# Kernel optimization log

Hardware: AMD Instinct MI355X
Metric: run time of the kernel (lower is better)

## Reference

```python
import jax, jax.numpy as jnp
import numpy as np

EMBED_DIM = 1024
NUM_HEADS = 16
HEAD_DIM = EMBED_DIM // NUM_HEADS
BITS = 8


def quantize_bits(x, bits):
    # Faithful min-max fake quantization from the original module.
    qmax = 2 ** bits - 1
    x_min = x.min()
    x_max = x.max()
    scale = (x_max - x_min) / (qmax + 1e-08)
    x_q = jnp.round(jnp.clip((x - x_min) / (scale + 1e-08), 0, qmax))
    return x_q * scale + x_min


def rope_sin_cos(seq_len, dim):
    # inv_freq over half the head dim, matching RotaryEmbedding's freqs table.
    inv_freq = 1.0 / 10000 ** (jnp.arange(0, dim, 2, dtype=jnp.float32) / dim)
    t = jnp.arange(seq_len, dtype=jnp.float32)
    freqs = t[:, None] * inv_freq[None, :]  # (S, D/2)
    return jnp.sin(freqs), jnp.cos(freqs)


def apply_rotary(x, sin, cos):
    # x: (B, H, S, D); sin/cos: (1, 1, S, D/2)
    x1, x2 = jnp.split(x, 2, axis=-1)
    return jnp.concatenate([x1 * cos - x2 * sin, x1 * sin + x2 * cos], axis=-1)


def setup_inputs() -> dict:
    key = jax.random.key(0)
    k1, k2, k3 = jax.random.split(key, 3)
    B, S, E = 2, 2048, EMBED_DIM
    x = jax.random.normal(k1, (B, S, E), dtype=jnp.float32)
    # lecun_normal-style init: std = 1/sqrt(fan_in)
    w_qkv = jax.random.normal(k2, (E, 3 * E), dtype=jnp.float32) / np.sqrt(E)
    w_out = jax.random.normal(k3, (E, E), dtype=jnp.float32) / np.sqrt(E)
    return {"x": x, "w_qkv": w_qkv, "w_out": w_out}


def reference(x, w_qkv, w_out):
    B, S, E = x.shape
    H, D = NUM_HEADS, HEAD_DIM
    # Fake-quantized QKV projection
    qkv = x @ quantize_bits(w_qkv, BITS)                    # (B, S, 3E)
    qkv = qkv.reshape(B, S, 3, H, D)
    q = qkv[:, :, 0].transpose(0, 2, 1, 3)                  # (B, H, S, D)
    k = qkv[:, :, 1].transpose(0, 2, 1, 3)
    v = qkv[:, :, 2].transpose(0, 2, 1, 3)
    sin, cos = rope_sin_cos(S, D)
    sin = sin[None, None]
    cos = cos[None, None]
    q = apply_rotary(q, sin, cos)
    k = apply_rotary(k, sin, cos)
    scores = jnp.einsum('bhqd,bhkd->bhqk', q, k) / jnp.sqrt(jnp.float32(D))
    attn = jax.nn.softmax(scores, axis=-1)                  # (B, H, S, S)
    out = jnp.einsum('bhqk,bhkd->bhqd', attn, v)            # (B, H, S, D)
    out = out.transpose(0, 2, 1, 3).reshape(B, S, E)
    return out @ quantize_bits(w_out, BITS)
```

## Files before the change

### kernel.cpp

```cpp
#include <hip/hip_runtime.h>
#include <hip/hip_bf16.h>

typedef __bf16 bf16;
typedef bf16  bf16x8 __attribute__((ext_vector_type(8)));
typedef bf16  bf16x4 __attribute__((ext_vector_type(4)));
typedef bf16  bf16x2 __attribute__((ext_vector_type(2)));
typedef float f32x4  __attribute__((ext_vector_type(4)));
typedef float f32x16 __attribute__((ext_vector_type(16)));
typedef int   i32x4  __attribute__((ext_vector_type(4)));

#define MFMA16(a,b,c) __builtin_amdgcn_mfma_f32_16x16x32_bf16((a),(b),(c),0,0,0)
#define MFMA32(a,b,c) __builtin_amdgcn_mfma_f32_32x32x16_bf16((a),(b),(c),0,0,0)

#define GLDS16(gp, lp) __builtin_amdgcn_global_load_lds( \
    (const __attribute__((address_space(1))) void*)(void*)(gp), \
    (__attribute__((address_space(3))) void*)(lp), 16, 0, 0)

static __device__ __forceinline__ bf16x8 lds_frag(const char* p){
  i32x4 v = *(const i32x4*)p;
  return __builtin_bit_cast(bf16x8, v);
}
static __device__ __forceinline__ bf16x8 g_frag(const bf16* p){
  i32x4 v = *(const i32x4*)p;
  return __builtin_bit_cast(bf16x8, v);
}
static __device__ __forceinline__ unsigned pk_bf16(float a, float b){
  bf16x2 v = { (bf16)a, (bf16)b };
  return __builtin_bit_cast(unsigned, v);
}
static __device__ __forceinline__ void p32swap(unsigned &a, unsigned &b){
  asm("v_permlane32_swap_b32 %0, %1" : "+v"(a), "+v"(b));
}

__device__ __forceinline__ unsigned fmap(float f){
  unsigned u = __float_as_uint(f);
  return (u & 0x80000000u) ? ~u : (u | 0x80000000u);
}
__device__ __forceinline__ float funmap(unsigned m){
  unsigned u = (m & 0x80000000u) ? (m & 0x7FFFFFFFu) : ~m;
  return __uint_as_float(u);
}

__global__ void init_mm(unsigned* mm){
  if (threadIdx.x == 0){
    mm[0] = 0xFFFFFFFFu; mm[1] = 0u;
    mm[2] = 0xFFFFFFFFu; mm[3] = 0u;
  }
}

__global__ void minmax_k(const float* __restrict__ w, int n, unsigned* __restrict__ mm){
  __shared__ unsigned smn[256], smx[256];
  int tid = threadIdx.x;
  unsigned lmn = 0xFFFFFFFFu, lmx = 0u;
  for (int i = blockIdx.x * blockDim.x + tid; i < n; i += gridDim.x * blockDim.x){
    unsigned u = fmap(w[i]);
    lmn = min(lmn, u); lmx = max(lmx, u);
  }
  smn[tid] = lmn; smx[tid] = lmx;
  __syncthreads();
  for (int s = 128; s > 0; s >>= 1){
    if (tid < s){
      smn[tid] = min(smn[tid], smn[tid + s]);
      smx[tid] = max(smx[tid], smx[tid + s]);
    }
    __syncthreads();
  }
  if (tid == 0){ atomicMin(&mm[0], smn[0]); atomicMax(&mm[1], smx[0]); }
}

__global__ void dq_t(const float* __restrict__ w, bf16* __restrict__ wt,
                     int R, int C, const unsigned* __restrict__ mm){
  __shared__ float t[32][33];
  float xmin = funmap(mm[0]);
  float xmax = funmap(mm[1]);
  float scale = (xmax - xmin) / 255.0f;
  float denom = scale + 1e-8f;
  int ct = blockIdx.x * 32, rt = blockIdx.y * 32;
  int tx = threadIdx.x, ty = threadIdx.y;
#pragma unroll
  for (int p = 0; p < 4; ++p){
    int r = rt + p * 8 + ty;
    float x = w[(size_t)r * C + ct + tx];
    float q = rintf(fminf(fmaxf((x - xmin) / denom, 0.0f), 255.0f));
    t[p * 8 + ty][tx] = q * scale + xmin;
  }
  __syncthreads();
#pragma unroll
  for (int p = 0; p < 4; ++p){
    int c = p * 8 + ty;
    wt[(size_t)(ct + c) * R + rt + tx] = (bf16)t[tx][c];
  }
}

__global__ void cast_x(const float* __restrict__ x, bf16* __restrict__ xb, int n4){
  int i = blockIdx.x * 256 + threadIdx.x;
  if (i < n4){
    f32x4 v = *(const f32x4*)(x + (size_t)i * 4);
    bf16x4 o = { (bf16)v.x, (bf16)v.y, (bf16)v.z, (bf16)v.w };
    *(bf16x4*)(xb + (size_t)i * 4) = o;
  }
}

__global__ void sincos_k(float2* __restrict__ sctab){
  int idx = blockIdx.x * 256 + threadIdx.x;
  int i = idx & 31, s = idx >> 5;
  float invf = powf(10000.0f, -(float)i / 32.0f);
  float fr = (float)s * invf;
  float2 cs; cs.x = cosf(fr); cs.y = sinf(fr);
  sctab[idx] = cs;
}

__global__ void vtrans_b(const bf16* __restrict__ Vraw, bf16* __restrict__ Vt){
  __shared__ float t[64][65];
  int bh = blockIdx.x >> 5;
  int st = (blockIdx.x & 31) * 64;
  int tx = threadIdx.x & 63, ty4 = threadIdx.x >> 6;
#pragma unroll
  for (int p = 0; p < 16; ++p){
    int s = p * 4 + ty4;
    t[s][tx] = (float)Vraw[((size_t)bh * 2048 + st + s) * 64 + tx];
  }
  __syncthreads();
#pragma unroll
  for (int p = 0; p < 16; ++p){
    int d = p * 4 + ty4;
    Vt[((size_t)bh * 64 + d) * 2048 + st + tx] = (bf16)t[tx][d];
  }
}

__global__ __launch_bounds__(256, 2) void gemm_bt(
    const bf16* __restrict__ A, const bf16* __restrict__ Bt,
    float* __restrict__ C, int M, int N, int K)
{
  __shared__ __align__(16) char lds[32768];
  int nbx = N >> 7;
  int bid = blockIdx.x;
  int nwg = gridDim.x;
  if ((nwg & 7) == 0){ int q = nwg >> 3; bid = (bid & 7) * q + (bid >> 3); }
  int row0 = (bid / nbx) << 7;
  int col0 = (bid % nbx) << 7;
  int tid = threadIdx.x, lane = tid & 63, wid = tid >> 6;
  int wr = (wid >> 1) * 64, wc = (wid & 1) * 64;
  int lr = lane & 15, g = lane >> 4;

  int aoff[2][4], boff[2][4];
#pragma unroll
  for (int kk = 0; kk < 2; ++kk){
#pragma unroll
    for (int m = 0; m < 4; ++m){
      int ra = wr + m * 16 + lr;
      aoff[kk][m] = ra * 128 + ((((kk * 4 + g) ^ ((ra >> 1) & 7))) << 4);
      int rb = wc + m * 16 + lr;
      boff[kk][m] = 16384 + rb * 128 + ((((kk * 4 + g) ^ ((rb >> 1) & 7))) << 4);
    }
  }

  const bf16* pA[4]; const bf16* pB[4]; int loff[4];
#pragma unroll
  for (int is = 0; is < 4; ++is){
    int f = is * 4096 + wid * 1024 + lane * 16;
    int r = f >> 7, c = (f >> 4) & 7;
    int cg = c ^ ((r >> 1) & 7);
    pA[is] = A  + (size_t)(row0 + r) * K + cg * 8;
    pB[is] = Bt + (size_t)(col0 + r) * K + cg * 8;
    loff[is] = is * 4096 + wid * 1024;
  }

  f32x4 acc[4][4] = {};
  for (int kt = 0; kt < K; kt += 64){
    __syncthreads();
#pragma unroll
    for (int is = 0; is < 4; ++is){
      GLDS16(pA[is] + kt, lds + loff[is]);
      GLDS16(pB[is] + kt, lds + 16384 + loff[is]);
    }
    __syncthreads();
#pragma unroll
    for (int kk = 0; kk < 2; ++kk){
      bf16x8 af[4], bfb[4];
#pragma unroll
      for (int m = 0; m < 4; ++m) af[m] = lds_frag(lds + aoff[kk][m]);
#pragma unroll
      for (int n = 0; n < 4; ++n) bfb[n] = lds_frag(lds + boff[kk][n]);
#pragma unroll
      for (int m = 0; m < 4; ++m)
#pragma unroll
        for (int n = 0; n < 4; ++n)
          acc[m][n] = MFMA16(af[m], bfb[n], acc[m][n]);
    }
  }

#pragma unroll
  for (int m = 0; m < 4; ++m){
    int row = row0 + wr + m * 16 + g * 4;
#pragma unroll
    for (int n = 0; n < 4; ++n){
      int col = col0 + wc + n * 16 + lr;
      float* cp = C + (size_t)row * N + col;
#pragma unroll
      for (int r = 0; r < 4; ++r)
        cp[(size_t)r * N] = acc[m][n][r];
    }
  }
}

__global__ __launch_bounds__(256, 2) void gemm_qkv(
    const bf16* __restrict__ A, const bf16* __restrict__ Bt,
    const float2* __restrict__ sctab,
    bf16* __restrict__ Qr, bf16* __restrict__ Kr, bf16* __restrict__ Vraw,
    int M, int N, int K)
{
  __shared__ __align__(16) char lds[32768];
  int nbx = N >> 7;
  int bid = blockIdx.x;
  int nwg = gridDim.x;
  if ((nwg & 7) == 0){ int q = nwg >> 3; bid = (bid & 7) * q + (bid >> 3); }
  int row0 = (bid / nbx) << 7;
  int col0 = (bid % nbx) << 7;
  int tid = threadIdx.x, lane = tid & 63, wid = tid >> 6;
  int wr = (wid >> 1) * 64, wc = (wid & 1) * 64;
  int lr = lane & 15, g = lane >> 4;

  int aoff[2][4], boff[2][4];
#pragma unroll
  for (int kk = 0; kk < 2; ++kk){
#pragma unroll
    for (int m = 0; m < 4; ++m){
      int ra = wr + m * 16 + lr;
      aoff[kk][m] = ra * 128 + ((((kk * 4 + g) ^ ((ra >> 1) & 7))) << 4);
      int rb = wc + m * 16 + lr;
      boff[kk][m] = 16384 + rb * 128 + ((((kk * 4 + g) ^ ((rb >> 1) & 7))) << 4);
    }
  }

  const bf16* pA[4]; const bf16* pB[4]; int loff[4];
#pragma unroll
  for (int is = 0; is < 4; ++is){
    int f = is * 4096 + wid * 1024 + lane * 16;
    int r = f >> 7, c = (f >> 4) & 7;
    int cg = c ^ ((r >> 1) & 7);
    pA[is] = A  + (size_t)(row0 + r) * K + cg * 8;
    pB[is] = Bt + (size_t)(col0 + r) * K + cg * 8;
    loff[is] = is * 4096 + wid * 1024;
  }

  f32x4 acc[4][4] = {};
  for (int kt = 0; kt < K; kt += 64){
    __syncthreads();
#pragma unroll
    for (int is = 0; is < 4; ++is){
      GLDS16(pA[is] + kt, lds + loff[is]);
      GLDS16(pB[is] + kt, lds + 16384 + loff[is]);
    }
    __syncthreads();
#pragma unroll
    for (int kk = 0; kk < 2; ++kk){
      bf16x8 af[4], bfb[4];
#pragma unroll
      for (int m = 0; m < 4; ++m) af[m] = lds_frag(lds + aoff[kk][m]);
#pragma unroll
      for (int n = 0; n < 4; ++n) bfb[n] = lds_frag(lds + boff[kk][n]);
#pragma unroll
      for (int m = 0; m < 4; ++m)
#pragma unroll
        for (int n = 0; n < 4; ++n)
          acc[m][n] = MFMA16(af[m], bfb[n], acc[m][n]);
    }
  }

  int head = (col0 + wc) >> 6;
  int sect = head >> 4;
  int h = head & 15;
  const float QS = 0.18033688011f;

  if (sect == 2){
#pragma unroll
    for (int m = 0; m < 4; ++m){
#pragma unroll
      for (int r = 0; r < 4; ++r){
        int s = row0 + wr + m * 16 + g * 4 + r;
        int b = s >> 11, s2 = s & 2047;
        bf16* vp = Vraw + (((size_t)(b * 16 + h)) * 2048 + s2) * 64;
#pragma unroll
        for (int n = 0; n < 4; ++n)
          vp[n * 16 + lr] = (bf16)acc[m][n][r];
      }
    }
  } else {
    bf16* dst = sect ? Kr : Qr;
    float scl = sect ? 1.0f : QS;
#pragma unroll
    for (int m = 0; m < 4; ++m){
#pragma unroll
      for (int r = 0; r < 4; ++r){
        int s = row0 + wr + m * 16 + g * 4 + r;
        int b = s >> 11, s2 = s & 2047;
        bf16* qp = dst + (((size_t)(b * 16 + h)) * 2048 + s2) * 64;
#pragma unroll
        for (int n = 0; n < 2; ++n){
          float x1 = acc[m][n][r], x2 = acc[m][n + 2][r];
          float2 cs = sctab[s2 * 32 + n * 16 + lr];
          qp[n * 16 + lr]      = (bf16)((x1 * cs.x - x2 * cs.y) * scl);
          qp[n * 16 + lr + 32] = (bf16)((x1 * cs.y + x2 * cs.x) * scl);
        }
      }
    }
  }
}

__global__ __launch_bounds__(256, 4) void attn_k(
    const bf16* __restrict__ Q, const bf16* __restrict__ K,
    const bf16* __restrict__ Vt, bf16* __restrict__ AO)
{
  __shared__ __align__(16) char SB[32768];
  __shared__ float mlds[4][2][32];
  __shared__ float invL[2][32];

  int bid = blockIdx.x;
  bid = (bid & 7) * 128 + (bid >> 3);
  int bh = bid >> 5, qb = bid & 31;
  int b = bh >> 4, h = bh & 15;
  int tid = threadIdx.x, lane = tid & 63, wid = tid >> 6;
  int l31 = lane & 31, hi = lane >> 5, hi8 = hi * 8;
  int qt = wid >> 1, half = wid & 1;
  int q0 = qb * 64 + qt * 32;

  const bf16* Qb = Q  + ((size_t)bh * 2048 + q0) * 64;
  const bf16* Kb = K  + (size_t)bh * 2048 * 64;
  const bf16* Vb = Vt + (size_t)bh * 64 * 2048;
  const bf16* Kh = Kb + (size_t)half * 1024 * 64;
  int vcol0 = half * 1024;

  bf16x8 qf[4];
#pragma unroll
  for (int t = 0; t < 4; ++t)
    qf[t] = g_frag(Qb + (size_t)l31 * 64 + t * 16 + hi8);

  const bf16* pKs[4]; const bf16* pVs[4]; int ldo[4];
#pragma unroll
  for (int is = 0; is < 4; ++is){
    int f = qt * 4096 + is * 1024 + lane * 16;
    int r = f >> 7;
    int cg = ((f >> 4) & 7) ^ (r & 7);
    pKs[is] = Kh + (size_t)r * 64 + cg * 8;
    pVs[is] = Vb + (size_t)r * 2048 + vcol0 + cg * 8;
    ldo[is] = qt * 4096 + is * 1024;
  }
  char* klh = SB + half * 8192;
  char* vlh = SB + 16384 + half * 8192;

  f32x16 o0 = {}, o1 = {};
  float mrun = -1e30f, lrun = 0.0f;

  for (int c = 0; c < 16; ++c){
    int kv0 = c * 64;
    __syncthreads();
#pragma unroll
    for (int is = 0; is < 4; ++is){
      GLDS16(pKs[is] + (size_t)kv0 * 64, klh + ldo[is]);
      GLDS16(pVs[is] + kv0,              vlh + ldo[is]);
    }
    __syncthreads();

#pragma unroll
    for (int kk = 0; kk < 2; ++kk){
      int krow = kk * 32 + l31;
      bf16x8 kf[4], vfr[4];
#pragma unroll
      for (int t = 0; t < 4; ++t)
        kf[t] = lds_frag(klh + krow * 128 + ((((2 * t + hi) ^ (krow & 7))) << 4));
#pragma unroll
      for (int u = 0; u < 4; ++u){
        int d = (u & 1) * 32 + l31;
        vfr[u] = lds_frag(vlh + d * 128 +
                          ((((kk * 4) + ((u >> 1) * 2) + hi) ^ (d & 7)) << 4));
      }
      f32x16 sc = {};
#pragma unroll
      for (int t = 0; t < 4; ++t) sc = MFMA32(kf[t], qf[t], sc);

      float a0 = fmaxf(sc[0], sc[1]),   a1 = fmaxf(sc[2], sc[3]);
      float a2 = fmaxf(sc[4], sc[5]),   a3 = fmaxf(sc[6], sc[7]);
      float a4 = fmaxf(sc[8], sc[9]),   a5 = fmaxf(sc[10], sc[11]);
      float a6 = fmaxf(sc[12], sc[13]), a7 = fmaxf(sc[14], sc[15]);
      a0 = fmaxf(a0, a1); a2 = fmaxf(a2, a3);
      a4 = fmaxf(a4, a5); a6 = fmaxf(a6, a7);
      float mt = fmaxf(fmaxf(a0, a2), fmaxf(a4, a6));
      if (!__all(mt - mrun <= 8.0f)){
        mt = fmaxf(mt, __shfl_xor(mt, 32));
        float mn = fmaxf(mrun, mt);
        float cr = __builtin_amdgcn_exp2f(mrun - mn);
#pragma unroll
        for (int r = 0; r < 16; ++r){ o0[r] *= cr; o1[r] *= cr; }
        lrun *= cr; mrun = mn;
      }
#pragma unroll
      for (int r = 0; r < 16; ++r) sc[r] = __builtin_amdgcn_exp2f(sc[r] - mrun);
      float s0 = (sc[0] + sc[1]) + (sc[2] + sc[3]);
      float s1 = (sc[4] + sc[5]) + (sc[6] + sc[7]);
      float s2 = (sc[8] + sc[9]) + (sc[10] + sc[11]);
      float s3 = (sc[12] + sc[13]) + (sc[14] + sc[15]);
      lrun += (s0 + s1) + (s2 + s3);

#pragma unroll
      for (int kh = 0; kh < 2; ++kh){
        unsigned pa0 = pk_bf16(sc[kh * 8 + 0], sc[kh * 8 + 1]);
        unsigned pa1 = pk_bf16(sc[kh * 8 + 2], sc[kh * 8 + 3]);
        unsigned pb0 = pk_bf16(sc[kh * 8 + 4], sc[kh * 8 + 5]);
        unsigned pb1 = pk_bf16(sc[kh * 8 + 6], sc[kh * 8 + 7]);
        p32swap(pa0, pb0); p32swap(pa1, pb1);
        i32x4 wv = { (int)pa0, (int)pa1, (int)pb0, (int)pb1 };
        bf16x8 pf = __builtin_bit_cast(bf16x8, wv);
        o0 = MFMA32(vfr[kh * 2 + 0], pf, o0);
        o1 = MFMA32(vfr[kh * 2 + 1], pf, o1);
      }
    }
  }

  lrun += __shfl_xor(lrun, 32);

  __syncthreads();
  if (lane < 32){ mlds[wid][0][l31] = mrun; mlds[wid][1][l31] = lrun; }
  __syncthreads();
  float mp = mlds[wid ^ 1][0][l31];
  float M = fmaxf(mrun, mp);
  float ew = __builtin_amdgcn_exp2f(mrun - M);
  if (half == 0 && lane < 32){
    float lp = mlds[wid ^ 1][1][l31];
    invL[qt][l31] = 1.0f / (lrun * ew + lp * __builtin_amdgcn_exp2f(mp - M));
  }
  float* Ow = (float*)SB + wid * 2048;
#pragma unroll
  for (int r = 0; r < 16; ++r){
    int d = 8 * (r >> 2) + 4 * hi + (r & 3);
    Ow[d * 32 + l31]        = o0[r] * ew;
    Ow[(d + 32) * 32 + l31] = o1[r] * ew;
  }
  __syncthreads();
  int qt2 = tid >> 7, qf31 = tid & 31, dseg = (tid >> 5) & 3;
  const float* Oa = (float*)SB + (2 * qt2) * 2048;
  const float* Ob = (float*)SB + (2 * qt2 + 1) * 2048;
  float iL = invL[qt2][qf31];
  bf16* outp = AO + ((size_t)(b * 2048 + qb * 64 + qt2 * 32 + qf31)) * 1024
                  + h * 64 + dseg * 16;
  bf16x8 w0, w1;
#pragma unroll
  for (int j = 0; j < 8; ++j){
    int d = dseg * 16 + j;
    w0[j] = (bf16)((Oa[d * 32 + qf31] + Ob[d * 32 + qf31]) * iL);
  }
#pragma unroll
  for (int j = 0; j < 8; ++j){
    int d = dseg * 16 + 8 + j;
    w1[j] = (bf16)((Oa[d * 32 + qf31] + Ob[d * 32 + qf31]) * iL);
  }
  *(bf16x8*)outp = w0;
  *(bf16x8*)(outp + 8) = w1;
}

extern "C" void kernel_launch(void* const* d_in, const int* in_sizes, int n_in,
                              void* d_out, int out_size, void* d_ws, size_t ws_size,
                              hipStream_t stream) {
  const float* x     = (const float*)d_in[0];
  const float* w_qkv = (const float*)d_in[1];
  const float* w_out = (const float*)d_in[2];
  float* out = (float*)d_out;

  char* ws = (char*)d_ws;
  const size_t MB = 1u << 20;
  unsigned* mm   = (unsigned*)(ws);
  float2* sctab  = (float2*)(ws + 256);
  bf16* xb       = (bf16*)(ws + 1 * MB);
  bf16* wqkvT    = (bf16*)(ws + 9 * MB);
  bf16* woutT    = (bf16*)(ws + 15 * MB);
  bf16* Vraw     = (bf16*)(ws + 17 * MB);
  bf16* Qr       = (bf16*)(ws + 65 * MB);
  bf16* Kr       = (bf16*)(ws + 73 * MB);
  bf16* Vt       = (bf16*)(ws + 81 * MB);
  bf16* AO       = (bf16*)(ws + 1 * MB);

  init_mm<<<1, 64, 0, stream>>>(mm);
  minmax_k<<<512, 256, 0, stream>>>(w_qkv, 1024 * 3072, mm);
  minmax_k<<<512, 256, 0, stream>>>(w_out, 1024 * 1024, mm + 2);
  sincos_k<<<256, 256, 0, stream>>>(sctab);
  cast_x<<<4096, 256, 0, stream>>>(x, xb, 4194304 / 4);
  dq_t<<<dim3(96, 32), dim3(32, 8), 0, stream>>>(w_qkv, wqkvT, 1024, 3072, mm);
  dq_t<<<dim3(32, 32), dim3(32, 8), 0, stream>>>(w_out, woutT, 1024, 1024, mm + 2);
  gemm_qkv<<<768, 256, 0, stream>>>(xb, wqkvT, sctab, Qr, Kr, Vraw, 4096, 3072, 1024);
  vtrans_b<<<1024, 256, 0, stream>>>(Vraw, Vt);
  attn_k<<<1024, 256, 0, stream>>>(Qr, Kr, Vt, AO);
  gemm_bt<<<256, 256, 0, stream>>>(AO, woutT, out, 4096, 1024, 1024);

  (void)in_sizes; (void)n_in; (void)out_size; (void)ws_size;
}
```

Before: 163.0 us.

## Write V transposed directly from QKV GEMM epilogue and drop transpose kernel

```diff
diff --git a/kernel.cpp b/kernel.cpp
--- a/kernel.cpp
+++ b/kernel.cpp
@@ -30,6 +30,9 @@
 }
 static __device__ __forceinline__ void p32swap(unsigned &a, unsigned &b){
   asm("v_permlane32_swap_b32 %0, %1" : "+v"(a), "+v"(b));
+}
+static __device__ __forceinline__ float max3(float a, float b, float c){
+  return fmaxf(fmaxf(a, b), c);
 }
 
 __device__ __forceinline__ unsigned fmap(float f){
@@ -108,24 +111,6 @@
   float fr = (float)s * invf;
   float2 cs; cs.x = cosf(fr); cs.y = sinf(fr);
   sctab[idx] = cs;
-}
-
-__global__ void vtrans_b(const bf16* __restrict__ Vraw, bf16* __restrict__ Vt){
-  __shared__ float t[64][65];
-  int bh = blockIdx.x >> 5;
-  int st = (blockIdx.x & 31) * 64;
-  int tx = threadIdx.x & 63, ty4 = threadIdx.x >> 6;
-#pragma unroll
-  for (int p = 0; p < 16; ++p){
-    int s = p * 4 + ty4;
-    t[s][tx] = (float)Vraw[((size_t)bh * 2048 + st + s) * 64 + tx];
-  }
-  __syncthreads();
-#pragma unroll
-  for (int p = 0; p < 16; ++p){
-    int d = p * 4 + ty4;
-    Vt[((size_t)bh * 64 + d) * 2048 + st + tx] = (bf16)t[tx][d];
-  }
 }
 
 __global__ __launch_bounds__(256, 2) void gemm_bt(
@@ -207,7 +192,7 @@
 __global__ __launch_bounds__(256, 2) void gemm_qkv(
     const bf16* __restrict__ A, const bf16* __restrict__ Bt,
     const float2* __restrict__ sctab,
-    bf16* __restrict__ Qr, bf16* __restrict__ Kr, bf16* __restrict__ Vraw,
+    bf16* __restrict__ Qr, bf16* __restrict__ Kr, bf16* __restrict__ Vt,
     int M, int N, int K)
 {
   __shared__ __align__(16) char lds[32768];
@@ -276,14 +261,14 @@
   if (sect == 2){
 #pragma unroll
     for (int m = 0; m < 4; ++m){
-#pragma unroll
-      for (int r = 0; r < 4; ++r){
-        int s = row0 + wr + m * 16 + g * 4 + r;
-        int b = s >> 11, s2 = s & 2047;
-        bf16* vp = Vraw + (((size_t)(b * 16 + h)) * 2048 + s2) * 64;
-#pragma unroll
-        for (int n = 0; n < 4; ++n)
-          vp[n * 16 + lr] = (bf16)acc[m][n][r];
+      int s = row0 + wr + m * 16 + g * 4;
+      int b = s >> 11, s2 = s & 2047;
+#pragma unroll
+      for (int n = 0; n < 4; ++n){
+        int d = n * 16 + lr;
+        bf16x4 v4 = { (bf16)acc[m][n][0], (bf16)acc[m][n][1],
+                      (bf16)acc[m][n][2], (bf16)acc[m][n][3] };
+        *(bf16x4*)(Vt + (((size_t)(b * 16 + h)) * 64 + d) * 2048 + s2) = v4;
       }
     }
   } else {
@@ -313,8 +298,6 @@
     const bf16* __restrict__ Vt, bf16* __restrict__ AO)
 {
   __shared__ __align__(16) char SB[32768];
-  __shared__ float mlds[4][2][32];
-  __shared__ float invL[2][32];
 
   int bid = blockIdx.x;
   bid = (bid & 7) * 128 + (bid >> 3);
@@ -379,13 +362,12 @@
 #pragma unroll
       for (int t = 0; t < 4; ++t) sc = MFMA32(kf[t], qf[t], sc);
 
-      float a0 = fmaxf(sc[0], sc[1]),   a1 = fmaxf(sc[2], sc[3]);
-      float a2 = fmaxf(sc[4], sc[5]),   a3 = fmaxf(sc[6], sc[7]);
-      float a4 = fmaxf(sc[8], sc[9]),   a5 = fmaxf(sc[10], sc[11]);
-      float a6 = fmaxf(sc[12], sc[13]), a7 = fmaxf(sc[14], sc[15]);
-      a0 = fmaxf(a0, a1); a2 = fmaxf(a2, a3);
-      a4 = fmaxf(a4, a5); a6 = fmaxf(a6, a7);
-      float mt = fmaxf(fmaxf(a0, a2), fmaxf(a4, a6));
+      float t0 = max3(sc[0], sc[1], sc[2]);
+      float t1 = max3(sc[3], sc[4], sc[5]);
+      float t2 = max3(sc[6], sc[7], sc[8]);
+      float t3 = max3(sc[9], sc[10], sc[11]);
+      float t4 = max3(sc[12], sc[13], sc[14]);
+      float mt = fmaxf(max3(t0, t1, t2), max3(t3, t4, sc[15]));
       if (!__all(mt - mrun <= 8.0f)){
         mt = fmaxf(mt, __shfl_xor(mt, 32));
         float mn = fmaxf(mrun, mt);
@@ -420,39 +402,39 @@
   lrun += __shfl_xor(lrun, 32);
 
   __syncthreads();
-  if (lane < 32){ mlds[wid][0][l31] = mrun; mlds[wid][1][l31] = lrun; }
-  __syncthreads();
-  float mp = mlds[wid ^ 1][0][l31];
+  float* ml = (float*)SB;
+  if (lane < 32){ ml[wid * 64 + l31] = mrun; ml[wid * 64 + 32 + l31] = lrun; }
+  __syncthreads();
+  float mp = ml[(wid ^ 1) * 64 + l31];
+  float lp = ml[(wid ^ 1) * 64 + 32 + l31];
+  __syncthreads();
   float M = fmaxf(mrun, mp);
   float ew = __builtin_amdgcn_exp2f(mrun - M);
-  if (half == 0 && lane < 32){
-    float lp = mlds[wid ^ 1][1][l31];
-    invL[qt][l31] = 1.0f / (lrun * ew + lp * __builtin_amdgcn_exp2f(mp - M));
-  }
+  float ep = __builtin_amdgcn_exp2f(mp - M);
+  float inv = ew / (lrun * ew + lp * ep);
   float* Ow = (float*)SB + wid * 2048;
 #pragma unroll
   for (int r = 0; r < 16; ++r){
     int d = 8 * (r >> 2) + 4 * hi + (r & 3);
-    Ow[d * 32 + l31]        = o0[r] * ew;
-    Ow[(d + 32) * 32 + l31] = o1[r] * ew;
+    Ow[d * 32 + l31]        = o0[r] * inv;
+    Ow[(d + 32) * 32 + l31] = o1[r] * inv;
   }
   __syncthreads();
   int qt2 = tid >> 7, qf31 = tid & 31, dseg = (tid >> 5) & 3;
   const float* Oa = (float*)SB + (2 * qt2) * 2048;
   const float* Ob = (float*)SB + (2 * qt2 + 1) * 2048;
-  float iL = invL[qt2][qf31];
   bf16* outp = AO + ((size_t)(b * 2048 + qb * 64 + qt2 * 32 + qf31)) * 1024
                   + h * 64 + dseg * 16;
   bf16x8 w0, w1;
 #pragma unroll
   for (int j = 0; j < 8; ++j){
     int d = dseg * 16 + j;
-    w0[j] = (bf16)((Oa[d * 32 + qf31] + Ob[d * 32 + qf31]) * iL);
+    w0[j] = (bf16)(Oa[d * 32 + qf31] + Ob[d * 32 + qf31]);
   }
 #pragma unroll
   for (int j = 0; j < 8; ++j){
     int d = dseg * 16 + 8 + j;
-    w1[j] = (bf16)((Oa[d * 32 + qf31] + Ob[d * 32 + qf31]) * iL);
+    w1[j] = (bf16)(Oa[d * 32 + qf31] + Ob[d * 32 + qf31]);
   }
   *(bf16x8*)outp = w0;
   *(bf16x8*)(outp + 8) = w1;
@@ -473,7 +455,6 @@
   bf16* xb       = (bf16*)(ws + 1 * MB);
   bf16* wqkvT    = (bf16*)(ws + 9 * MB);
   bf16* woutT    = (bf16*)(ws + 15 * MB);
-  bf16* Vraw     = (bf16*)(ws + 17 * MB);
   bf16* Qr       = (bf16*)(ws + 65 * MB);
   bf16* Kr       = (bf16*)(ws + 73 * MB);
   bf16* Vt       = (bf16*)(ws + 81 * MB);
@@ -486,8 +467,7 @@
   cast_x<<<4096, 256, 0, stream>>>(x, xb, 4194304 / 4);
   dq_t<<<dim3(96, 32), dim3(32, 8), 0, stream>>>(w_qkv, wqkvT, 1024, 3072, mm);
   dq_t<<<dim3(32, 32), dim3(32, 8), 0, stream>>>(w_out, woutT, 1024, 1024, mm + 2);
-  gemm_qkv<<<768, 256, 0, stream>>>(xb, wqkvT, sctab, Qr, Kr, Vraw, 4096, 3072, 1024);
-  vtrans_b<<<1024, 256, 0, stream>>>(Vraw, Vt);
+  gemm_qkv<<<768, 256, 0, stream>>>(xb, wqkvT, sctab, Qr, Kr, Vt, 4096, 3072, 1024);
   attn_k<<<1024, 256, 0, stream>>>(Qr, Kr, Vt, AO);
   gemm_bt<<<256, 256, 0, stream>>>(AO, woutT, out, 4096, 1024, 1024);
 
```

Result: faster. 157.4 us (-3.4%).
